# Kernel tuning notes

Measured on AMD Instinct MI355X. Metric: run time of the kernel, lower is better.

The kernel has to match this reference:

```python
import jax, jax.numpy as jnp
import numpy as np

N, E, M = 20000, 320000, 64
LOG2 = float(np.log(2.0))
INV_SQRT_M = 1.0 / float(np.sqrt(M))
PW_S = float(np.sqrt(1.0 / 5.0))   # path weight for 0e-output paths: sqrt(ir_out.dim / n_paths)
PW_V = float(np.sqrt(3.0 / 5.0))   # path weight for 1e-output paths
INV_SQRT3 = 1.0 / float(np.sqrt(3.0))
INV_SQRT2 = 1.0 / float(np.sqrt(2.0))


def ssp(x):  # ShiftedSoftPlus
    return jax.nn.softplus(x) - LOG2


def split(feat):
    return feat[:, :M], feat[:, M:].reshape(feat.shape[0], M, 3)


def e3_linear(feat, W0, b0, W1):
    # e3nn o3.Linear per irrep group, fan-in normalized; bias only on scalar (0e) irreps
    s, v = split(feat)
    s = s @ (W0 * INV_SQRT_M) + b0
    v = jnp.einsum('nui,uv->nvi', v, W1 * INV_SQRT_M)
    return jnp.concatenate([s, v.reshape(v.shape[0], 3 * M)], axis=-1)


def fcnet(h, Ws):
    # e3nn FullyConnectedNet: no biases, fan-in normalized, ssp between layers
    for i, W in enumerate(Ws):
        h = h @ (W * (1.0 / float(np.sqrt(W.shape[0]))))
        if i < len(Ws) - 1:
            h = ssp(h)
    return h


def setup_inputs() -> dict:
    key = jax.random.key(0)
    ks = jax.random.split(key, 24)
    r = lambda i, shape: jax.random.normal(ks[i], shape, dtype=jnp.float32)
    inp = {
        'x': r(0, (N, 4 * M)),
        'edge_index': jax.random.randint(ks[1], (2, E), 0, N, dtype=jnp.int64)
        if jax.config.jax_enable_x64 else jax.random.randint(ks[1], (2, E), 0, N),
        'edge_sh': r(2, (E, 4)),
        'edge_attr': r(3, (E, 64)),
        # linear_node_pre
        'W_pre0': r(4, (M, M)), 'b_pre0': jnp.zeros((M,), jnp.float32), 'W_pre1': r(5, (M, M)),
        # NormGate fc (plain torch nn.Linear with bias)
        'Wg1': r(6, (2 * M, 2 * M)) * 0.08, 'bg1': jnp.zeros((2 * M,), jnp.float32),
        'Wg2': r(7, (2 * M, 2 * M)) * 0.08, 'bg2': jnp.zeros((2 * M,), jnp.float32),
        # linear_node
        'Wn0': r(8, (M, M)), 'bn0': jnp.zeros((M,), jnp.float32), 'Wn1': r(9, (M, M)),
        # fc_node: [edge_attr_dim=64, 32, weight_numel=5*M]
        'Wf1': r(10, (64, 32)), 'Wf2': r(11, (32, 5 * M)),
        # layer_l0: [192, 32, 5*M]
        'Wl1': r(12, (192, 32)), 'Wl2': r(13, (32, 5 * M)),
        # linear_out
        'Wo0': r(14, (M, M)), 'bo0': jnp.zeros((M,), jnp.float32), 'Wo1': r(15, (M, M)),
    }
    return inp


def reference(x, edge_index, edge_sh, edge_attr,
              W_pre0, b_pre0, W_pre1, Wg1, bg1, Wg2, bg2,
              Wn0, bn0, Wn1, Wf1, Wf2, Wl1, Wl2, Wo0, bo0, Wo1):
    edge_dst, edge_src = edge_index[0], edge_index[1]

    # --- pre linear + edge invariants s0 ---
    pre_x = e3_linear(x, W_pre0, b_pre0, W_pre1)
    ps, pv = split(pre_x)
    # InnerProduct on 1e group (uuu, path weight 1/ir.dim): mean over m of elementwise product
    ip1 = jnp.einsum('eui,eui->eu', pv[edge_dst], pv[edge_src]) * (1.0 / 3.0)  # [E, M]
    s0 = jnp.concatenate([ps[edge_dst], ps[edge_dst], ip1], axis=-1)  # [E, 192]

    # --- NormGate ---
    xs, xv = split(x)
    norm_v = jnp.sqrt(jnp.sum(xv * xv, axis=-1) + 1e-12)  # [N, M]
    f0 = jnp.concatenate([xs, norm_v], axis=-1)  # [N, 2M]
    g = jax.nn.silu(f0 @ Wg1 + bg1) @ Wg2 + bg2  # [N, 2M]
    gated = xv * g[:, M:, None]
    xg = jnp.concatenate([g[:, :M], gated.reshape(N, 3 * M)], axis=-1)

    xg = e3_linear(xg, Wn0, bn0, Wn1)
    self_x = xg

    # --- per-edge tensor product weights ---
    w = (fcnet(edge_attr, [Wf1, Wf2]) * fcnet(s0, [Wl1, Wl2])).reshape(E, 5, M)

    # --- edge-wise equivariant tensor product (uvu, 5 paths) ---
    gs, gv = split(xg)
    es, ev = gs[edge_src], gv[edge_src]            # [E,M], [E,M,3]
    sh0, sh1 = edge_sh[:, 0], edge_sh[:, 1:4]      # [E], [E,3]

    out_s = PW_S * (w[:, 0] * es * sh0[:, None]
                    + w[:, 3] * jnp.einsum('eui,ei->eu', ev, sh1) * INV_SQRT3)
    cross = jnp.cross(ev, sh1[:, None, :])
    out_v = PW_V * (w[:, 1][:, :, None] * es[:, :, None] * sh1[:, None, :]
                    + w[:, 2][:, :, None] * ev * sh0[:, None, None]
                    + w[:, 4][:, :, None] * cross * INV_SQRT2)
    edge_feat = jnp.concatenate([out_s, out_v.reshape(E, 3 * M)], axis=-1)  # [E, 4M]

    # --- scatter aggregate to destination nodes ---
    out = jax.ops.segment_sum(edge_feat, edge_dst, num_segments=N)
    out = out + self_x  # irrep_in_node == irrep_out
    out = e3_linear(out, Wo0, bo0, Wo1)
    return out
```

## Files before the change

kernel.cpp:

```cpp
#include <hip/hip_runtime.h>
#include <math.h>

#define NNODE 20000
#define NEDGE 320000

__device__ __forceinline__ float sspf(float x) {
    return fmaxf(x, 0.f) + log1pf(expf(-fabsf(x))) - 0.6931471805599453f;
}

__device__ __forceinline__ float rlf(float v, int l) {
    return __int_as_float(__builtin_amdgcn_readlane(__float_as_int(v), l));
}

__global__ __launch_bounds__(256) void k_e3lin(
    const float* __restrict__ in, const float* __restrict__ add,
    float* __restrict__ out,
    const float* __restrict__ W0, const float* __restrict__ b0,
    const float* __restrict__ W1, int nrows)
{
    __shared__ float sW0[64 * 64];
    __shared__ float sW1[64 * 64];
    __shared__ float sb0[64];
    __shared__ float srow[4][256];
    const int tid = threadIdx.x;
    for (int i = tid; i < 64 * 16; i += 256) {
        ((float4*)sW0)[i] = ((const float4*)W0)[i];
        ((float4*)sW1)[i] = ((const float4*)W1)[i];
    }
    if (tid < 64) sb0[tid] = b0[tid];
    __syncthreads();

    const int rr = tid >> 6;
    const int v  = tid & 63;
    for (int r0 = blockIdx.x * 4; r0 < nrows; r0 += gridDim.x * 4) {
        {
            int i = tid;
            int r = i >> 6, c = i & 63;
            int row = r0 + r;
            float4 val = make_float4(0.f, 0.f, 0.f, 0.f);
            if (row < nrows) {
                val = ((const float4*)(in + (size_t)row * 256))[c];
                if (add) {
                    float4 a = ((const float4*)(add + (size_t)row * 256))[c];
                    val.x += a.x; val.y += a.y; val.z += a.z; val.w += a.w;
                }
            }
            ((float4*)srow[r])[c] = val;
        }
        __syncthreads();

        int row = r0 + rr;
        if (row < nrows) {
            const float* rw = srow[rr];
            float s = 0.f, a0 = 0.f, a1 = 0.f, a2 = 0.f;
            #pragma unroll 16
            for (int u = 0; u < 64; ++u) {
                float w0 = sW0[u * 64 + v];
                float w1 = sW1[u * 64 + v];
                s  += rw[u] * w0;
                a0 += rw[64 + u * 3 + 0] * w1;
                a1 += rw[64 + u * 3 + 1] * w1;
                a2 += rw[64 + u * 3 + 2] * w1;
            }
            out[row * 256 + v]              = s  * 0.125f + sb0[v];
            out[row * 256 + 64 + v * 3 + 0] = a0 * 0.125f;
            out[row * 256 + 64 + v * 3 + 1] = a1 * 0.125f;
            out[row * 256 + 64 + v * 3 + 2] = a2 * 0.125f;
        }
        __syncthreads();
    }
}

__global__ __launch_bounds__(256) void k_gate(
    const float* __restrict__ x, float* __restrict__ xg,
    const float* __restrict__ Wg1, const float* __restrict__ bg1,
    const float* __restrict__ Wg2, const float* __restrict__ bg2,
    int nrows)
{
    __shared__ float sW1[128 * 128];
    __shared__ float sW2[128 * 128];
    __shared__ float sb1[128], sb2[128];
    __shared__ float srow[2][256];
    __shared__ float sf0[2][128];
    __shared__ float sh1[2][128];
    const int tid = threadIdx.x;
    for (int i = tid; i < 128 * 32; i += 256) {
        ((float4*)sW1)[i] = ((const float4*)Wg1)[i];
        ((float4*)sW2)[i] = ((const float4*)Wg2)[i];
    }
    if (tid < 128) { sb1[tid] = bg1[tid]; sb2[tid] = bg2[tid]; }
    __syncthreads();

    const int rr = tid >> 7;
    const int j  = tid & 127;
    for (int base = blockIdx.x * 2; base < nrows; base += gridDim.x * 2) {
        if (tid < 128) {
            int r = tid >> 6, c = tid & 63;
            int row = base + r;
            float4 v = make_float4(0.f, 0.f, 0.f, 0.f);
            if (row < nrows) v = ((const float4*)(x + (size_t)row * 256))[c];
            ((float4*)srow[r])[c] = v;
        }
        __syncthreads();
        {
            float f;
            if (j < 64) f = srow[rr][j];
            else {
                int u = j - 64;
                float v0 = srow[rr][64 + u * 3 + 0];
                float v1 = srow[rr][64 + u * 3 + 1];
                float v2 = srow[rr][64 + u * 3 + 2];
                f = sqrtf(v0 * v0 + v1 * v1 + v2 * v2 + 1e-12f);
            }
            sf0[rr][j] = f;
        }
        __syncthreads();
        {
            float acc = sb1[j];
            #pragma unroll 16
            for (int k = 0; k < 128; ++k) acc += sf0[rr][k] * sW1[k * 128 + j];
            sh1[rr][j] = acc / (1.f + expf(-acc));
        }
        __syncthreads();
        {
            float acc = sb2[j];
            #pragma unroll 16
            for (int k = 0; k < 128; ++k) acc += sh1[rr][k] * sW2[k * 128 + j];
            int row = base + rr;
            if (row < nrows) {
                if (j < 64) xg[row * 256 + j] = acc;
                else {
                    int u = j - 64;
                    xg[row * 256 + 64 + u * 3 + 0] = srow[rr][64 + u * 3 + 0] * acc;
                    xg[row * 256 + 64 + u * 3 + 1] = srow[rr][64 + u * 3 + 1] * acc;
                    xg[row * 256 + 64 + u * 3 + 2] = srow[rr][64 + u * 3 + 2] * acc;
                }
            }
        }
        __syncthreads();
    }
}

__global__ __launch_bounds__(256) void k_hist(const int* __restrict__ ei, int* __restrict__ hist) {
    int e = blockIdx.x * 256 + threadIdx.x;
    if (e < NEDGE) atomicAdd(&hist[ei[e]], 1);
}

__global__ __launch_bounds__(1024) void k_scan(const int* __restrict__ hist,
                                               int* __restrict__ offs,
                                               int* __restrict__ curs) {
    __shared__ int part[1024];
    const int t = threadIdx.x;
    const int base = t * 20;
    int loc[20];
    int s = 0;
    #pragma unroll
    for (int k = 0; k < 20; ++k) {
        int b = base + k;
        int v = (b < NNODE) ? hist[b] : 0;
        loc[k] = s; s += v;
    }
    part[t] = s;
    __syncthreads();
    for (int off = 1; off < 1024; off <<= 1) {
        int v = (t >= off) ? part[t - off] : 0;
        __syncthreads();
        part[t] += v;
        __syncthreads();
    }
    int excl = (t == 0) ? 0 : part[t - 1];
    #pragma unroll
    for (int k = 0; k < 20; ++k) {
        int b = base + k;
        if (b < NNODE) { offs[b] = excl + loc[k]; curs[b] = excl + loc[k]; }
    }
    if (t == 1023) offs[NNODE] = part[1023];
}

__global__ __launch_bounds__(256) void k_scatteridx(const int* __restrict__ ei,
                                                    int* __restrict__ curs,
                                                    int* __restrict__ order) {
    int e = blockIdx.x * 256 + threadIdx.x;
    if (e < NEDGE) {
        int p = atomicAdd(&curs[ei[e]], 1);
        order[p] = e;
    }
}

#define EPW 4
__global__ __launch_bounds__(1024, 4) void k_edge(
    const float* __restrict__ pre, const float* __restrict__ slf,
    const int* __restrict__ ei, const float* __restrict__ eshp,
    const float* __restrict__ ea,
    const int* __restrict__ offs, const int* __restrict__ order,
    const float* __restrict__ Wf1, const float* __restrict__ Wf2,
    const float* __restrict__ Wl1, const float* __restrict__ Wl2,
    float* __restrict__ acc)
{
    __shared__ float2 sW1mb[64 * 64];
    __shared__ float4 sW2a[32 * 64];
    __shared__ float4 sW2b[32 * 64];
    __shared__ float2 sW2c[32 * 64];
    __shared__ float  sEAV[16][EPW][64];
    __shared__ float  sPSD[16][64];
    const int tid = threadIdx.x;
    const float sc_f1 = 0.125f;
    const float sc_l1 = 0.07216878364870323f;
    const float sc_2  = 0.17677669529663687f;
    for (int i = tid; i < 64 * 64; i += 1024) {
        int u = i >> 6, c = i & 63, j = c & 31;
        float wm, wb;
        if (c < 32) {
            wm = Wf1[u * 32 + j] * sc_f1;
            wb = 0.f;
        } else {
            wm = (Wl1[u * 32 + j] + Wl1[(64 + u) * 32 + j]) * sc_l1;
            wb = Wl1[(128 + u) * 32 + j] * sc_l1;
        }
        sW1mb[i] = make_float2(wm, wb);
    }
    for (int i = tid; i < 32 * 64; i += 1024) {
        int jj = i >> 6, col = i & 63;
        const float* f2 = Wf2 + jj * 320 + col;
        const float* l2 = Wl2 + jj * 320 + col;
        sW2a[i] = make_float4(f2[0] * sc_2, f2[64] * sc_2, f2[128] * sc_2, f2[192] * sc_2);
        sW2b[i] = make_float4(l2[0] * sc_2, l2[64] * sc_2, l2[128] * sc_2, l2[192] * sc_2);
        sW2c[i] = make_float2(f2[256] * sc_2, l2[256] * sc_2);
    }
    __syncthreads();

    const int lane  = tid & 63;
    const int w     = tid >> 6;
    const int gwave = blockIdx.x * (blockDim.x >> 6) + w;
    const int nwav  = gridDim.x * (blockDim.x >> 6);
    const bool lo   = (lane < 32);

    const float* inbp[EPW];
    #pragma unroll
    for (int t = 0; t < EPW; ++t)
        inbp[t] = lo ? &sEAV[w][t][0] : &sPSD[w][0];

    const float PW_S = 0.4472135954999579f;
    const float PW_V = 0.7745966692414834f;
    const float IS3  = 0.5773502691896258f;
    const float IS2  = 0.7071067811865476f;

    for (int d = gwave; d < NNODE; d += nwav) {
        const int e0 = __builtin_amdgcn_readfirstlane(offs[d]);
        const int e1 = __builtin_amdgcn_readfirstlane(offs[d + 1]);
        float psd = pre[d * 256 + lane];
        float pd0 = pre[d * 256 + 64 + lane * 3 + 0];
        float pd1 = pre[d * 256 + 64 + lane * 3 + 1];
        float pd2 = pre[d * 256 + 64 + lane * 3 + 2];
        sPSD[w][lane] = psd;

        float accS = 0.f, aV0 = 0.f, aV1 = 0.f, aV2 = 0.f;

        for (int i = e0; i < e1; i += EPW) {
            const int cnt = e1 - i;
            int eo[EPW], srcv[EPW];
            float ip1[EPW];
            #pragma unroll
            for (int t = 0; t < EPW; ++t) {
                int idx = (t < cnt) ? (i + t) : i;
                int e = __builtin_amdgcn_readfirstlane(order[idx]);
                int s = __builtin_amdgcn_readfirstlane(ei[NEDGE + e]);
                eo[t] = e; srcv[t] = s;
                float ps0 = pre[s * 256 + 64 + lane * 3 + 0];
                float ps1 = pre[s * 256 + 64 + lane * 3 + 1];
                float ps2 = pre[s * 256 + 64 + lane * 3 + 2];
                ip1[t] = (pd0 * ps0 + pd1 * ps1 + pd2 * ps2) * (1.f / 3.f);
                sEAV[w][t][lane] = ea[e * 64 + lane];
            }

            float hacc[EPW] = {0.f, 0.f, 0.f, 0.f};
            #pragma unroll 16
            for (int uu = 0; uu < 64; ++uu) {
                float2 wmb = sW1mb[uu * 64 + lane];
                #pragma unroll
                for (int t = 0; t < EPW; ++t) {
                    float b1 = inbp[t][uu];
                    float bI = rlf(ip1[t], uu);
                    hacc[t] += b1 * wmb.x + bI * wmb.y;
                }
            }
            float hval[EPW];
            #pragma unroll
            for (int t = 0; t < EPW; ++t) hval[t] = sspf(hacc[t]);

            float aA[EPW][5], aB[EPW][5];
            #pragma unroll
            for (int t = 0; t < EPW; ++t)
                #pragma unroll
                for (int k = 0; k < 5; ++k) { aA[t][k] = 0.f; aB[t][k] = 0.f; }
            #pragma unroll 8
            for (int jj = 0; jj < 32; ++jj) {
                float4 wa = sW2a[jj * 64 + lane];
                float4 wb = sW2b[jj * 64 + lane];
                float2 wc = sW2c[jj * 64 + lane];
                #pragma unroll
                for (int t = 0; t < EPW; ++t) {
                    float hA = rlf(hval[t], jj);
                    float hB = rlf(hval[t], jj + 32);
                    aA[t][0] += hA * wa.x; aA[t][1] += hA * wa.y;
                    aA[t][2] += hA * wa.z; aA[t][3] += hA * wa.w;
                    aA[t][4] += hA * wc.x;
                    aB[t][0] += hB * wb.x; aB[t][1] += hB * wb.y;
                    aB[t][2] += hB * wb.z; aB[t][3] += hB * wb.w;
                    aB[t][4] += hB * wc.y;
                }
            }

            #pragma unroll
            for (int t = 0; t < EPW; ++t) {
                if (t >= cnt) break;
                int e = eo[t], s = srcv[t];
                float w0 = aA[t][0] * aB[t][0];
                float w1 = aA[t][1] * aB[t][1];
                float w2 = aA[t][2] * aB[t][2];
                float w3 = aA[t][3] * aB[t][3];
                float w4 = aA[t][4] * aB[t][4];
                float es  = slf[s * 256 + lane];
                float ev0 = slf[s * 256 + 64 + lane * 3 + 0];
                float ev1 = slf[s * 256 + 64 + lane * 3 + 1];
                float ev2 = slf[s * 256 + 64 + lane * 3 + 2];
                float s0v = eshp[e * 4 + 0];
                float sx  = eshp[e * 4 + 1];
                float sy  = eshp[e * 4 + 2];
                float sz  = eshp[e * 4 + 3];
                float dotv = ev0 * sx + ev1 * sy + ev2 * sz;
                accS += PW_S * (w0 * es * s0v + w3 * dotv * IS3);
                float cx = ev1 * sz - ev2 * sy;
                float cy = ev2 * sx - ev0 * sz;
                float cz = ev0 * sy - ev1 * sx;
                aV0 += PW_V * (w1 * es * sx + w2 * ev0 * s0v + w4 * cx * IS2);
                aV1 += PW_V * (w1 * es * sy + w2 * ev1 * s0v + w4 * cy * IS2);
                aV2 += PW_V * (w1 * es * sz + w2 * ev2 * s0v + w4 * cz * IS2);
            }
        }

        acc[d * 256 + lane]              = accS;
        acc[d * 256 + 64 + lane * 3 + 0] = aV0;
        acc[d * 256 + 64 + lane * 3 + 1] = aV1;
        acc[d * 256 + 64 + lane * 3 + 2] = aV2;
    }
}

extern "C" void kernel_launch(void* const* d_in, const int* in_sizes, int n_in,
                              void* d_out, int out_size, void* d_ws, size_t ws_size,
                              hipStream_t stream) {
    const float* x     = (const float*)d_in[0];
    const int*   ei    = (const int*)  d_in[1];
    const float* esh   = (const float*)d_in[2];
    const float* eattr = (const float*)d_in[3];
    const float* Wpre0 = (const float*)d_in[4];
    const float* bpre0 = (const float*)d_in[5];
    const float* Wpre1 = (const float*)d_in[6];
    const float* Wg1   = (const float*)d_in[7];
    const float* bg1   = (const float*)d_in[8];
    const float* Wg2   = (const float*)d_in[9];
    const float* bg2   = (const float*)d_in[10];
    const float* Wn0   = (const float*)d_in[11];
    const float* bn0   = (const float*)d_in[12];
    const float* Wn1   = (const float*)d_in[13];
    const float* Wf1   = (const float*)d_in[14];
    const float* Wf2   = (const float*)d_in[15];
    const float* Wl1   = (const float*)d_in[16];
    const float* Wl2   = (const float*)d_in[17];
    const float* Wo0   = (const float*)d_in[18];
    const float* bo0   = (const float*)d_in[19];
    const float* Wo1   = (const float*)d_in[20];
    float* out = (float*)d_out;
    float* ws  = (float*)d_ws;

    float* pre = ws;
    float* xg  = ws + (size_t)NNODE * 256;
    float* slf = ws + (size_t)NNODE * 256 * 2;
    float* acc = ws + (size_t)NNODE * 256 * 3;
    int*   hist  = (int*)(ws + (size_t)NNODE * 256 * 4);
    int*   offs  = hist + NNODE;
    int*   curs  = offs + NNODE + 2;
    int*   order = curs + NNODE;

    hipMemsetAsync(hist, 0, NNODE * sizeof(int), stream);
    k_hist      <<<(NEDGE + 255) / 256, 256, 0, stream>>>(ei, hist);
    k_scan      <<<1, 1024, 0, stream>>>(hist, offs, curs);
    k_scatteridx<<<(NEDGE + 255) / 256, 256, 0, stream>>>(ei, curs, order);

    k_e3lin<<<1280, 256, 0, stream>>>(x,  nullptr, pre, Wpre0, bpre0, Wpre1, NNODE);
    k_gate <<<512,  256, 0, stream>>>(x,  xg, Wg1, bg1, Wg2, bg2, NNODE);
    k_e3lin<<<1280, 256, 0, stream>>>(xg, nullptr, slf, Wn0, bn0, Wn1, NNODE);
    k_edge <<<256, 1024, 0, stream>>>(pre, slf, ei, esh, eattr, offs, order,
                                      Wf1, Wf2, Wl1, Wl2, acc);
    k_e3lin<<<1280, 256, 0, stream>>>(acc, slf, out, Wo0, bo0, Wo1, NNODE);
}
```

Baseline: 1.178 ms.

## Pack edge MLP weights as bf16 in LDS, raise occupancy, add dynamic node scheduling

The per-edge MLP weights in shared memory are stored as packed bfloat16 pairs instead of fp32, roughly halving LDS footprint so more blocks can be resident. Launch bounds and grid size are doubled to use that extra occupancy, and the static grid-stride node loop is replaced by an atomic work counter to balance nodes with uneven in-degree. The trade-offs are reduced weight precision, extra unpacking ALU work, more register pressure under the tighter launch bound, and one global atomic per node.

```diff
diff --git a/kernel.cpp b/kernel.cpp
--- a/kernel.cpp
+++ b/kernel.cpp
@@ -11,6 +11,16 @@
 __device__ __forceinline__ float rlf(float v, int l) {
     return __int_as_float(__builtin_amdgcn_readlane(__float_as_int(v), l));
 }
+
+__device__ __forceinline__ unsigned int bfp(float x) {
+    unsigned int b = __float_as_uint(x);
+    return (b + 0x7fffu + ((b >> 16) & 1u)) >> 16;
+}
+__device__ __forceinline__ unsigned int pk2(float lo, float hi) {
+    return bfp(lo) | (bfp(hi) << 16);
+}
+__device__ __forceinline__ float ulo(unsigned int u) { return __uint_as_float(u << 16); }
+__device__ __forceinline__ float uhi(unsigned int u) { return __uint_as_float(u & 0xffff0000u); }
 
 __global__ __launch_bounds__(256) void k_e3lin(
     const float* __restrict__ in, const float* __restrict__ add,
@@ -188,19 +198,19 @@
 }
 
 #define EPW 4
-__global__ __launch_bounds__(1024, 4) void k_edge(
+__global__ __launch_bounds__(1024, 8) void k_edge(
     const float* __restrict__ pre, const float* __restrict__ slf,
     const int* __restrict__ ei, const float* __restrict__ eshp,
     const float* __restrict__ ea,
     const int* __restrict__ offs, const int* __restrict__ order,
     const float* __restrict__ Wf1, const float* __restrict__ Wf2,
     const float* __restrict__ Wl1, const float* __restrict__ Wl2,
-    float* __restrict__ acc)
+    float* __restrict__ acc, int* __restrict__ ctr)
 {
-    __shared__ float2 sW1mb[64 * 64];
-    __shared__ float4 sW2a[32 * 64];
-    __shared__ float4 sW2b[32 * 64];
-    __shared__ float2 sW2c[32 * 64];
+    __shared__ unsigned int sW1mb[64 * 64];
+    __shared__ uint2        sW2a [32 * 64];
+    __shared__ uint2        sW2b [32 * 64];
+    __shared__ unsigned int sW2c [32 * 64];
     __shared__ float  sEAV[16][EPW][64];
     __shared__ float  sPSD[16][64];
     const int tid = threadIdx.x;
@@ -217,23 +227,23 @@
             wm = (Wl1[u * 32 + j] + Wl1[(64 + u) * 32 + j]) * sc_l1;
             wb = Wl1[(128 + u) * 32 + j] * sc_l1;
         }
-        sW1mb[i] = make_float2(wm, wb);
+        sW1mb[i] = pk2(wm, wb);
     }
     for (int i = tid; i < 32 * 64; i += 1024) {
         int jj = i >> 6, col = i & 63;
         const float* f2 = Wf2 + jj * 320 + col;
         const float* l2 = Wl2 + jj * 320 + col;
-        sW2a[i] = make_float4(f2[0] * sc_2, f2[64] * sc_2, f2[128] * sc_2, f2[192] * sc_2);
-        sW2b[i] = make_float4(l2[0] * sc_2, l2[64] * sc_2, l2[128] * sc_2, l2[192] * sc_2);
-        sW2c[i] = make_float2(f2[256] * sc_2, l2[256] * sc_2);
+        sW2a[i] = make_uint2(pk2(f2[0] * sc_2, f2[64] * sc_2),
+                             pk2(f2[128] * sc_2, f2[192] * sc_2));
+        sW2b[i] = make_uint2(pk2(l2[0] * sc_2, l2[64] * sc_2),
+                             pk2(l2[128] * sc_2, l2[192] * sc_2));
+        sW2c[i] = pk2(f2[256] * sc_2, l2[256] * sc_2);
     }
     __syncthreads();
 
-    const int lane  = tid & 63;
-    const int w     = tid >> 6;
-    const int gwave = blockIdx.x * (blockDim.x >> 6) + w;
-    const int nwav  = gridDim.x * (blockDim.x >> 6);
-    const bool lo   = (lane < 32);
+    const int lane = tid & 63;
+    const int w    = tid >> 6;
+    const bool lo  = (lane < 32);
 
     const float* inbp[EPW];
     #pragma unroll
@@ -245,7 +255,12 @@
     const float IS3  = 0.5773502691896258f;
     const float IS2  = 0.7071067811865476f;
 
-    for (int d = gwave; d < NNODE; d += nwav) {
+    for (;;) {
+        int dv = 0;
+        if (lane == 0) dv = atomicAdd(ctr, 1);
+        const int d = __builtin_amdgcn_readfirstlane(dv);
+        if (d >= NNODE) break;
+
         const int e0 = __builtin_amdgcn_readfirstlane(offs[d]);
         const int e1 = __builtin_amdgcn_readfirstlane(offs[d + 1]);
         float psd = pre[d * 256 + lane];
@@ -276,12 +291,13 @@
             float hacc[EPW] = {0.f, 0.f, 0.f, 0.f};
             #pragma unroll 16
             for (int uu = 0; uu < 64; ++uu) {
-                float2 wmb = sW1mb[uu * 64 + lane];
+                unsigned int wmb = sW1mb[uu * 64 + lane];
+                float wm = ulo(wmb), wb = uhi(wmb);
                 #pragma unroll
                 for (int t = 0; t < EPW; ++t) {
                     float b1 = inbp[t][uu];
                     float bI = rlf(ip1[t], uu);
-                    hacc[t] += b1 * wmb.x + bI * wmb.y;
+                    hacc[t] += b1 * wm + bI * wb;
                 }
             }
             float hval[EPW];
@@ -295,19 +311,22 @@
                 for (int k = 0; k < 5; ++k) { aA[t][k] = 0.f; aB[t][k] = 0.f; }
             #pragma unroll 8
             for (int jj = 0; jj < 32; ++jj) {
-                float4 wa = sW2a[jj * 64 + lane];
-                float4 wb = sW2b[jj * 64 + lane];
-                float2 wc = sW2c[jj * 64 + lane];
+                uint2 ua = sW2a[jj * 64 + lane];
+                uint2 ub = sW2b[jj * 64 + lane];
+                unsigned int uc = sW2c[jj * 64 + lane];
+                float wa0 = ulo(ua.x), wa1 = uhi(ua.x), wa2 = ulo(ua.y), wa3 = uhi(ua.y);
+                float wb0 = ulo(ub.x), wb1 = uhi(ub.x), wb2 = ulo(ub.y), wb3 = uhi(ub.y);
+                float wa4 = ulo(uc),   wb4 = uhi(uc);
                 #pragma unroll
                 for (int t = 0; t < EPW; ++t) {
                     float hA = rlf(hval[t], jj);
                     float hB = rlf(hval[t], jj + 32);
-                    aA[t][0] += hA * wa.x; aA[t][1] += hA * wa.y;
-                    aA[t][2] += hA * wa.z; aA[t][3] += hA * wa.w;
-                    aA[t][4] += hA * wc.x;
-                    aB[t][0] += hB * wb.x; aB[t][1] += hB * wb.y;
-                    aB[t][2] += hB * wb.z; aB[t][3] += hB * wb.w;
-                    aB[t][4] += hB * wc.y;
+                    aA[t][0] += hA * wa0; aA[t][1] += hA * wa1;
+                    aA[t][2] += hA * wa2; aA[t][3] += hA * wa3;
+                    aA[t][4] += hA * wa4;
+                    aB[t][0] += hB * wb0; aB[t][1] += hB * wb1;
+                    aB[t][2] += hB * wb2; aB[t][3] += hB * wb3;
+                    aB[t][4] += hB * wb4;
                 }
             }
 
@@ -381,8 +400,10 @@
     int*   offs  = hist + NNODE;
     int*   curs  = offs + NNODE + 2;
     int*   order = curs + NNODE;
+    int*   ctr   = order + NEDGE;
 
     hipMemsetAsync(hist, 0, NNODE * sizeof(int), stream);
+    hipMemsetAsync(ctr, 0, sizeof(int), stream);
     k_hist      <<<(NEDGE + 255) / 256, 256, 0, stream>>>(ei, hist);
     k_scan      <<<1, 1024, 0, stream>>>(hist, offs, curs);
     k_scatteridx<<<(NEDGE + 255) / 256, 256, 0, stream>>>(ei, curs, order);
@@ -390,7 +411,7 @@
     k_e3lin<<<1280, 256, 0, stream>>>(x,  nullptr, pre, Wpre0, bpre0, Wpre1, NNODE);
     k_gate <<<512,  256, 0, stream>>>(x,  xg, Wg1, bg1, Wg2, bg2, NNODE);
     k_e3lin<<<1280, 256, 0, stream>>>(xg, nullptr, slf, Wn0, bn0, Wn1, NNODE);
-    k_edge <<<256, 1024, 0, stream>>>(pre, slf, ei, esh, eattr, offs, order,
-                                      Wf1, Wf2, Wl1, Wl2, acc);
+    k_edge <<<512, 1024, 0, stream>>>(pre, slf, ei, esh, eattr, offs, order,
+                                      Wf1, Wf2, Wl1, Wl2, acc, ctr);
     k_e3lin<<<1280, 256, 0, stream>>>(acc, slf, out, Wo0, bo0, Wo1, NNODE);
 }
```

After: 2.166 ms. +83.8%, slower.
